# Optimization experiments

Hardware: AMD Instinct MI355X
Metric: run time of the kernel (lower is better)

The kernel has to match this reference:

```python
import jax, jax.numpy as jnp
import numpy as np

# Equal-capacity grouped-GEMM view of megablocks SparseMLP:
# tokens are pre-sorted by expert; topo's block-sparsity is equivalent to a
# per-expert dense GEMM over that expert's token slice.
E, T, H, F = 8, 2048, 1024, 4096  # experts, tokens/expert, hidden, ffn_hidden


def setup_inputs() -> dict:
    key = jax.random.key(0)
    k1, k2, k3 = jax.random.split(key, 3)
    x = jax.random.normal(k1, (E, T, H), dtype=jnp.float32)
    w1 = jax.random.normal(k2, (E, F, H), dtype=jnp.float32) * 0.02
    w2 = jax.random.normal(k3, (E, F, H), dtype=jnp.float32) * 0.02
    return {"x": x, "w1": w1, "w2": w2}


def reference(x, w1, w2):
    # sdd(x, w1.t(), topo): per-expert x_e @ w1_e^T -> [E, T, F]
    h = jnp.einsum('eth,efh->etf', x, w1)
    # megablocks DEFAULT_ACTIVATION_FN = gelu(approximate='tanh')
    a = jax.nn.gelu(h, approximate=True)
    # dsd(act, w2): per-expert a_e @ w2_e -> [E, T, H]
    return jnp.einsum('etf,efh->eth', a, w2)
```

## Files before the change

kernel.cpp:

```cpp
#include <hip/hip_runtime.h>
#include <hip/hip_bf16.h>


typedef __bf16 bf16x8 __attribute__((ext_vector_type(8)));
typedef float  f32x16 __attribute__((ext_vector_type(16)));

__device__ inline unsigned short f2b(float f) {
    unsigned u = __float_as_uint(f);
    u += 0x7fff + ((u >> 16) & 1);
    return (unsigned short)(u >> 16);
}

__global__ void cast_f32_bf16(const float* __restrict__ in,
                              unsigned short* __restrict__ out, int n4) {
    int i = blockIdx.x * 256 + threadIdx.x;
    if (i >= n4) return;
    float4 v = ((const float4*)in)[i];
    ushort4 o;
    o.x = f2b(v.x); o.y = f2b(v.y); o.z = f2b(v.z); o.w = f2b(v.w);
    ((ushort4*)out)[i] = o;
}

__global__ void transpose_cast(const float* __restrict__ in,
                               unsigned short* __restrict__ out, int F, int H) {
    __shared__ float tile[64][33];
    const int e = blockIdx.z;
    const int f0 = blockIdx.y * 64, h0 = blockIdx.x * 32;
    const float* src = in + (long long)e * F * H;
    unsigned short* dst = out + (long long)e * F * H;
    const int tx = threadIdx.x, ty = threadIdx.y;
#pragma unroll
    for (int i = 0; i < 64; i += 8)
        tile[ty + i][tx] = src[(long long)(f0 + ty + i) * H + h0 + tx];
    __syncthreads();
#pragma unroll
    for (int i = 0; i < 32; i += 8) {
        const int h = ty + i;
        ushort2 o;
        o.x = f2b(tile[2 * tx][h]);
        o.y = f2b(tile[2 * tx + 1][h]);
        *(ushort2*)&dst[(long long)(h0 + h) * F + f0 + 2 * tx] = o;
    }
}

template <bool GELU, bool RASTER1D, typename CT>
__global__ __launch_bounds__(256) void gemm_bt(
    const unsigned short* __restrict__ A,
    const unsigned short* __restrict__ B,
    CT* __restrict__ C, int M, int N, int K) {
    int e, bm, bn;
    if constexpr (RASTER1D) {
        const int id = blockIdx.x;
        const int xcd = id & 7, s = id >> 3, t = s & 15;
        e  = s >> 4;
        bm = (xcd * 2 + (t >> 3)) * 128;
        bn = (t & 7) * 128;
    } else {
        e = blockIdx.z; bm = blockIdx.y * 128; bn = blockIdx.x * 128;
    }
    A += (long long)e * M * K;
    B += (long long)e * N * K;
    C += (long long)e * M * N;

    __shared__ unsigned short sA[128 * 64];
    __shared__ unsigned short sB[128 * 64];

    const int tid  = threadIdx.x;
    const int lane = tid & 63;
    const int wave = tid >> 6;
    const int half = lane >> 5, r32 = lane & 31;
    const int wm = (wave & 1) * 64, wn = (wave >> 1) * 64;

    f32x16 acc[2][2] = {};

    for (int k0 = 0; k0 < K; k0 += 64) {
#pragma unroll
        for (int r = 0; r < 4; ++r) {
            const int eoff = r * 2048 + tid * 8;
            const int row = eoff >> 6;
            const int cD  = (eoff >> 3) & 7;
            const int scol = ((cD ^ (row & 7)) << 3);
            const unsigned short* ga = A + (long long)(bm + row) * K + k0 + scol;
            const unsigned short* gb = B + (long long)(bn + row) * K + k0 + scol;
            __builtin_amdgcn_global_load_lds(
                (const __attribute__((address_space(1))) void*)ga,
                (__attribute__((address_space(3))) void*)(&sA[eoff]), 16, 0, 0);
            __builtin_amdgcn_global_load_lds(
                (const __attribute__((address_space(1))) void*)gb,
                (__attribute__((address_space(3))) void*)(&sB[eoff]), 16, 0, 0);
        }
        __syncthreads();

#pragma unroll
        for (int ks = 0; ks < 4; ++ks) {
            bf16x8 af[2], bfr[2];
            const int cL = ks * 2 + half;
#pragma unroll
            for (int i = 0; i < 2; ++i) {
                const int ra = wm + i * 32 + r32;
                const int rb = wn + i * 32 + r32;
                af[i]  = *(const bf16x8*)&sA[ra * 64 + ((cL ^ (ra & 7)) << 3)];
                bfr[i] = *(const bf16x8*)&sB[rb * 64 + ((cL ^ (rb & 7)) << 3)];
            }
#pragma unroll
            for (int i = 0; i < 2; ++i)
#pragma unroll
                for (int j = 0; j < 2; ++j)
                    acc[i][j] = __builtin_amdgcn_mfma_f32_32x32x16_bf16(
                        af[i], bfr[j], acc[i][j], 0, 0, 0);
        }
        __syncthreads();
    }

#pragma unroll
    for (int i = 0; i < 2; ++i) {
        const int row_base = bm + wm + i * 32;
#pragma unroll
        for (int j = 0; j < 2; ++j) {
            const int col = bn + wn + j * 32 + r32;
#pragma unroll
            for (int r = 0; r < 16; ++r) {
                const int row = row_base + (r & 3) + 8 * (r >> 2) + 4 * half;
                float v = acc[i][j][r];
                if (GELU) {
                    float t = 1.5957691216057308f * (v + 0.044715f * v * v * v);
                    v = v / (1.0f + __expf(-t));
                }
                if constexpr (sizeof(CT) == 2) {
                    ((unsigned short*)C)[(long long)row * N + col] = f2b(v);
                } else {
                    ((float*)C)[(long long)row * N + col] = v;
                }
            }
        }
    }
}

extern "C" void kernel_launch(void* const* d_in, const int* in_sizes, int n_in,
                              void* d_out, int out_size, void* d_ws, size_t ws_size,
                              hipStream_t stream) {
    constexpr int E = 8, T = 2048, H = 1024, F = 4096;
    const float* x  = (const float*)d_in[0];
    const float* w1 = (const float*)d_in[1];
    const float* w2 = (const float*)d_in[2];
    float* out = (float*)d_out;

    unsigned short* xb  = (unsigned short*)d_ws;
    unsigned short* w1b = xb  + (size_t)E * T * H;
    unsigned short* w2t = w1b + (size_t)E * F * H;
    unsigned short* ab  = w2t + (size_t)E * F * H;

    const int nx = E * T * H / 4, nw = E * F * H / 4;
    cast_f32_bf16<<<(nx + 255) / 256, 256, 0, stream>>>(x, xb, nx);
    cast_f32_bf16<<<(nw + 255) / 256, 256, 0, stream>>>(w1, w1b, nw);
    transpose_cast<<<dim3(H / 32, F / 64, E), dim3(32, 8), 0, stream>>>(w2, w2t, F, H);

    gemm_bt<true, false, unsigned short>
        <<<dim3(F / 128, T / 128, E), 256, 0, stream>>>(xb, w1b, ab, T, F, H);
    gemm_bt<false, true, float>
        <<<dim3(E * (T / 128) * (H / 128)), 256, 0, stream>>>(ab, w2t, out, T, H, F);
}
```

Baseline: 686.0 us.

## Add double-buffered 256x256 GEMM kernel for second projection and fuse cast kernels

Introduces a new 512-thread GEMM kernel with 256x256 output tiles, double-buffered LDS staging via direct global-to-LDS loads, staggered prefetch of A and B interleaved with MFMA phases, and s_setprio hints. It is used for the long-K second GEMM, aiming to overlap loads with compute and raise data reuse per block. The x and w1 cast kernels are merged into one launch, and the first GEMM hoists its address math out of the K loop with a 3-waves occupancy hint. The manual vmcnt/lgkmcnt waits are easy to get wrong, the larger tile raises register pressure, and the tile count (256 blocks) matches the CU count with only one block per CU.

Measured after the change: 640.9 us. 6.6% less time.

```diff
diff --git a/kernel.cpp b/kernel.cpp
--- a/kernel.cpp
+++ b/kernel.cpp
@@ -11,14 +11,26 @@
     return (unsigned short)(u >> 16);
 }
 
-__global__ void cast_f32_bf16(const float* __restrict__ in,
-                              unsigned short* __restrict__ out, int n4) {
+__global__ void cast2_f32_bf16(const float* __restrict__ a,
+                               unsigned short* __restrict__ oa, int na4,
+                               const float* __restrict__ b,
+                               unsigned short* __restrict__ ob, int nb4) {
     int i = blockIdx.x * 256 + threadIdx.x;
-    if (i >= n4) return;
-    float4 v = ((const float4*)in)[i];
+    const float4* src;
+    ushort4* dst;
+    if (i < na4) {
+        src = (const float4*)a + i;
+        dst = (ushort4*)oa + i;
+    } else {
+        i -= na4;
+        if (i >= nb4) return;
+        src = (const float4*)b + i;
+        dst = (ushort4*)ob + i;
+    }
+    float4 v = *src;
     ushort4 o;
     o.x = f2b(v.x); o.y = f2b(v.y); o.z = f2b(v.z); o.w = f2b(v.w);
-    ((ushort4*)out)[i] = o;
+    *dst = o;
 }
 
 __global__ void transpose_cast(const float* __restrict__ in,
@@ -43,21 +55,13 @@
     }
 }
 
-template <bool GELU, bool RASTER1D, typename CT>
-__global__ __launch_bounds__(256) void gemm_bt(
+template <bool GELU, typename CT>
+__global__ __launch_bounds__(256, 3) void gemm_bt(
     const unsigned short* __restrict__ A,
     const unsigned short* __restrict__ B,
     CT* __restrict__ C, int M, int N, int K) {
-    int e, bm, bn;
-    if constexpr (RASTER1D) {
-        const int id = blockIdx.x;
-        const int xcd = id & 7, s = id >> 3, t = s & 15;
-        e  = s >> 4;
-        bm = (xcd * 2 + (t >> 3)) * 128;
-        bn = (t & 7) * 128;
-    } else {
-        e = blockIdx.z; bm = blockIdx.y * 128; bn = blockIdx.x * 128;
-    }
+    const int e = blockIdx.z;
+    const int bm = blockIdx.y * 128, bn = blockIdx.x * 128;
     A += (long long)e * M * K;
     B += (long long)e * N * K;
     C += (long long)e * M * N;
@@ -71,23 +75,31 @@
     const int half = lane >> 5, r32 = lane & 31;
     const int wm = (wave & 1) * 64, wn = (wave >> 1) * 64;
 
+    const unsigned short* ga[4];
+    const unsigned short* gb[4];
+#pragma unroll
+    for (int r = 0; r < 4; ++r) {
+        const int eoff = r * 2048 + tid * 8;
+        const int row = eoff >> 6;
+        const int cD  = (eoff >> 3) & 7;
+        const int scol = ((cD ^ (row & 7)) << 3);
+        ga[r] = A + (long long)(bm + row) * K + scol;
+        gb[r] = B + (long long)(bn + row) * K + scol;
+    }
+
     f32x16 acc[2][2] = {};
 
     for (int k0 = 0; k0 < K; k0 += 64) {
 #pragma unroll
         for (int r = 0; r < 4; ++r) {
             const int eoff = r * 2048 + tid * 8;
-            const int row = eoff >> 6;
-            const int cD  = (eoff >> 3) & 7;
-            const int scol = ((cD ^ (row & 7)) << 3);
-            const unsigned short* ga = A + (long long)(bm + row) * K + k0 + scol;
-            const unsigned short* gb = B + (long long)(bn + row) * K + k0 + scol;
             __builtin_amdgcn_global_load_lds(
-                (const __attribute__((address_space(1))) void*)ga,
+                (const __attribute__((address_space(1))) void*)ga[r],
                 (__attribute__((address_space(3))) void*)(&sA[eoff]), 16, 0, 0);
             __builtin_amdgcn_global_load_lds(
-                (const __attribute__((address_space(1))) void*)gb,
+                (const __attribute__((address_space(1))) void*)gb[r],
                 (__attribute__((address_space(3))) void*)(&sB[eoff]), 16, 0, 0);
+            ga[r] += 64; gb[r] += 64;
         }
         __syncthreads();
 
@@ -136,6 +148,204 @@
     }
 }
 
+#define STG(dst, ptr, q)                                                      \
+    __builtin_amdgcn_global_load_lds(                                         \
+        (const __attribute__((address_space(1))) void*)(ptr),                 \
+        (__attribute__((address_space(3))) void*)(&(dst)[(q) * 4096 + sdst]), \
+        16, 0, 0)
+#define LGK0 do { asm volatile("s_waitcnt lgkmcnt(0)" ::: "memory");          \
+                  __builtin_amdgcn_sched_barrier(0); } while (0)
+
+template <bool GELU, typename CT>
+__global__ __launch_bounds__(512) void gemm_ra(
+    const unsigned short* __restrict__ A,
+    const unsigned short* __restrict__ B,
+    CT* __restrict__ C, int M, int N, int K) {
+    const int nwg = gridDim.x;
+    const int id = blockIdx.x;
+    const int wgid = (id & 7) * (nwg >> 3) + (id >> 3);
+    const int ntn = N >> 8;
+    const int tpe = (M >> 8) * ntn;
+    const int e = wgid / tpe;
+    const int rem = wgid - e * tpe;
+    const int bm = (rem / ntn) << 8;
+    const int bn = (rem % ntn) << 8;
+    A += (long long)e * M * K;
+    B += (long long)e * N * K;
+    C += (long long)e * M * N;
+
+    __shared__ __align__(16) unsigned short sA[2][16384];
+    __shared__ __align__(16) unsigned short sB[2][16384];
+
+    const int tid = threadIdx.x;
+    const int lane = tid & 63;
+    const int wid = tid >> 6;
+    const int half = lane >> 5, r32 = lane & 31;
+    const int wm = (wid >> 2) * 128;
+    const int wn = (wid & 3) * 64;
+
+    const int srow = tid >> 3;
+    const int scol = ((tid & 7) ^ ((tid >> 3) & 7)) << 3;
+    const int sdst = tid * 8;
+
+    const unsigned short* pA[4];
+    const unsigned short* pB[4];
+#pragma unroll
+    for (int q = 0; q < 4; ++q) {
+        pA[q] = A + (long long)(bm + q * 64 + srow) * K + scol;
+        pB[q] = B + (long long)(bn + q * 64 + srow) * K + scol;
+    }
+    const int NT = K >> 6;
+
+    STG(sA[0], pA[0], 0); STG(sA[0], pA[1], 1);
+    STG(sA[0], pA[2], 2); STG(sA[0], pA[3], 3);
+    STG(sB[0], pB[0], 0); STG(sB[0], pB[1], 1);
+    STG(sB[0], pB[2], 2); STG(sB[0], pB[3], 3);
+    if (NT > 1) {
+#pragma unroll
+        for (int q = 0; q < 4; ++q) STG(sB[1], pB[q] + 64, q);
+        asm volatile("s_waitcnt vmcnt(4)" ::: "memory");
+    } else {
+        asm volatile("s_waitcnt vmcnt(0)" ::: "memory");
+    }
+#pragma unroll
+    for (int q = 0; q < 4; ++q) { pA[q] += 64; pB[q] += 128; }
+    __builtin_amdgcn_s_barrier();
+
+    f32x16 acc[4][2] = {};
+    bf16x8 af[2][4], bf0[4], bf1[4];
+
+#pragma unroll
+    for (int m = 0; m < 2; ++m) {
+        const int row = wm + m * 32 + r32;
+#pragma unroll
+        for (int ks = 0; ks < 4; ++ks)
+            af[m][ks] = *(const bf16x8*)
+                &sA[0][row * 64 + (((ks * 2 + half) ^ (row & 7)) << 3)];
+    }
+    {
+        const int row = wn + r32;
+#pragma unroll
+        for (int ks = 0; ks < 4; ++ks)
+            bf0[ks] = *(const bf16x8*)
+                &sB[0][row * 64 + (((ks * 2 + half) ^ (row & 7)) << 3)];
+    }
+
+    for (int kt = 0; kt < NT; ++kt) {
+        const int p = kt & 1;
+        const bool pfA = (kt + 1 < NT), pfB = (kt + 2 < NT);
+        unsigned short* nA = sA[p ^ 1];
+        unsigned short* stB = sB[p];
+
+        LGK0;
+        __builtin_amdgcn_s_setprio(1);
+#pragma unroll
+        for (int ks = 0; ks < 4; ++ks)
+#pragma unroll
+            for (int m = 0; m < 2; ++m)
+                acc[m][0] = __builtin_amdgcn_mfma_f32_32x32x16_bf16(
+                    af[m][ks], bf0[ks], acc[m][0], 0, 0, 0);
+        __builtin_amdgcn_s_setprio(0);
+        {
+            const int row = wn + 32 + r32;
+#pragma unroll
+            for (int ks = 0; ks < 4; ++ks)
+                bf1[ks] = *(const bf16x8*)
+                    &sB[p][row * 64 + (((ks * 2 + half) ^ (row & 7)) << 3)];
+        }
+        if (pfA) { STG(nA, pA[0], 0); STG(nA, pA[1], 1); }
+
+        LGK0;
+        __builtin_amdgcn_s_setprio(1);
+#pragma unroll
+        for (int ks = 0; ks < 4; ++ks)
+#pragma unroll
+            for (int m = 0; m < 2; ++m)
+                acc[m][1] = __builtin_amdgcn_mfma_f32_32x32x16_bf16(
+                    af[m][ks], bf1[ks], acc[m][1], 0, 0, 0);
+        __builtin_amdgcn_s_setprio(0);
+        if (pfA) { STG(nA, pA[2], 2); STG(nA, pA[3], 3); }
+        __builtin_amdgcn_s_barrier();
+
+#pragma unroll
+        for (int m = 0; m < 2; ++m) {
+            const int row = wm + 64 + m * 32 + r32;
+#pragma unroll
+            for (int ks = 0; ks < 4; ++ks)
+                af[m][ks] = *(const bf16x8*)
+                    &sA[p][row * 64 + (((ks * 2 + half) ^ (row & 7)) << 3)];
+        }
+        if (pfB) { STG(stB, pB[0], 0); STG(stB, pB[1], 1); }
+        LGK0;
+        __builtin_amdgcn_s_setprio(1);
+#pragma unroll
+        for (int ks = 0; ks < 4; ++ks)
+#pragma unroll
+            for (int m = 0; m < 2; ++m)
+                acc[2 + m][0] = __builtin_amdgcn_mfma_f32_32x32x16_bf16(
+                    af[m][ks], bf0[ks], acc[2 + m][0], 0, 0, 0);
+        __builtin_amdgcn_s_setprio(0);
+
+        __builtin_amdgcn_s_setprio(1);
+#pragma unroll
+        for (int ks = 0; ks < 4; ++ks)
+#pragma unroll
+            for (int m = 0; m < 2; ++m)
+                acc[2 + m][1] = __builtin_amdgcn_mfma_f32_32x32x16_bf16(
+                    af[m][ks], bf1[ks], acc[2 + m][1], 0, 0, 0);
+        __builtin_amdgcn_s_setprio(0);
+        if (pfB) { STG(stB, pB[2], 2); STG(stB, pB[3], 3); }
+        if (pfB) asm volatile("s_waitcnt vmcnt(4)" ::: "memory");
+        else     asm volatile("s_waitcnt vmcnt(0)" ::: "memory");
+        __builtin_amdgcn_s_barrier();
+
+        if (pfA) {
+            const unsigned short* cA = sA[p ^ 1];
+            const unsigned short* cB = sB[p ^ 1];
+#pragma unroll
+            for (int m = 0; m < 2; ++m) {
+                const int row = wm + m * 32 + r32;
+#pragma unroll
+                for (int ks = 0; ks < 4; ++ks)
+                    af[m][ks] = *(const bf16x8*)
+                        &cA[row * 64 + (((ks * 2 + half) ^ (row & 7)) << 3)];
+            }
+            const int row = wn + r32;
+#pragma unroll
+            for (int ks = 0; ks < 4; ++ks)
+                bf0[ks] = *(const bf16x8*)
+                    &cB[row * 64 + (((ks * 2 + half) ^ (row & 7)) << 3)];
+#pragma unroll
+            for (int q = 0; q < 4; ++q) { pA[q] += 64; pB[q] += 64; }
+        }
+    }
+
+#pragma unroll
+    for (int mb = 0; mb < 4; ++mb) {
+        const int row_base = bm + wm + mb * 32;
+#pragma unroll
+        for (int nb = 0; nb < 2; ++nb) {
+            const int col = bn + wn + nb * 32 + r32;
+#pragma unroll
+            for (int r = 0; r < 16; ++r) {
+                const int row = row_base + (r & 3) + 8 * (r >> 2) + 4 * half;
+                float v = acc[mb][nb][r];
+                if (GELU) {
+                    float t = 1.5957691216057308f * (v + 0.044715f * v * v * v);
+                    v = v / (1.0f + __expf(-t));
+                }
+                if constexpr (sizeof(CT) == 2) {
+                    ((unsigned short*)C)[(long long)row * N + col] = f2b(v);
+                } else {
+                    ((float*)C)[(long long)row * N + col] = v;
+                }
+            }
+        }
+    }
+}
+#undef STG
+#undef LGK0
+
 extern "C" void kernel_launch(void* const* d_in, const int* in_sizes, int n_in,
                               void* d_out, int out_size, void* d_ws, size_t ws_size,
                               hipStream_t stream) {
@@ -151,12 +361,11 @@
     unsigned short* ab  = w2t + (size_t)E * F * H;
 
     const int nx = E * T * H / 4, nw = E * F * H / 4;
-    cast_f32_bf16<<<(nx + 255) / 256, 256, 0, stream>>>(x, xb, nx);
-    cast_f32_bf16<<<(nw + 255) / 256, 256, 0, stream>>>(w1, w1b, nw);
+    cast2_f32_bf16<<<(nx + nw + 255) / 256, 256, 0, stream>>>(x, xb, nx, w1, w1b, nw);
     transpose_cast<<<dim3(H / 32, F / 64, E), dim3(32, 8), 0, stream>>>(w2, w2t, F, H);
 
-    gemm_bt<true, false, unsigned short>
+    gemm_bt<true, unsigned short>
         <<<dim3(F / 128, T / 128, E), 256, 0, stream>>>(xb, w1b, ab, T, F, H);
-    gemm_bt<false, true, float>
-        <<<dim3(E * (T / 128) * (H / 128)), 256, 0, stream>>>(ab, w2t, out, T, H, F);
-}
+    gemm_ra<false, float>
+        <<<dim3(E * (T / 256) * (H / 256)), 512, 0, stream>>>(ab, w2t, out, T, H, F);
+}
```
